# Kernel tuning notes

Hardware: AMD Instinct MI355X
Metric: run time of the kernel (lower is better)

The kernel has to match this reference:

```python
import jax, jax.numpy as jnp
import numpy as np

B, S, T, H, E, V = 64, 512, 12, 256, 256, 50000


def _xavier(key, shape):
    lim = np.sqrt(6.0 / (shape[0] + shape[1]))
    return jax.random.uniform(key, shape, jnp.float32, -lim, lim)


def setup_inputs() -> dict:
    key = jax.random.key(0)
    ks = jax.random.split(key, 14)
    return {
        "input_ids": jax.random.randint(ks[0], (B, S), 0, V),
        "tree_ids": jax.random.randint(ks[1], (B, T, S), 0, S),
        "tree_ids_r": jax.random.randint(ks[2], (B, T, S), 0, S),
        "tree_ids_l": jax.random.randint(ks[3], (B, T, S), 0, S),
        "emb": _xavier(ks[4], (V, E)),
        "W_ioux": _xavier(ks[5], (E, 3 * H)),
        "b_ioux": jnp.zeros((3 * H,), jnp.float32),
        "U_iou_r": _xavier(ks[6], (H, 3 * H)),
        "U_iou_l": _xavier(ks[7], (H, 3 * H)),
        "W_f": _xavier(ks[8], (E, H)),
        "b_f": jnp.zeros((H,), jnp.float32),
        "U_f0": _xavier(ks[9], (H, H)),
        "U_f1": _xavier(ks[10], (H, H)),
        "U_f2": _xavier(ks[11], (H, H)),
        "U_f3": _xavier(ks[12], (H, H)),
    }


def reference(input_ids, tree_ids, tree_ids_r, tree_ids_l, emb,
              W_ioux, b_ioux, U_iou_r, U_iou_l, W_f, b_f,
              U_f0, U_f1, U_f2, U_f3):
    x = emb[input_ids]                      # [B, S, E]
    Bn, Sn = x.shape[0], x.shape[1]
    Hn = U_f0.shape[0]
    bidx = jnp.arange(Bn)[:, None]          # [B, 1] batch index for scatter

    def take(a, idx):                       # gather along node dim: out[b,s]=a[b,idx[b,s]]
        return jnp.take_along_axis(a, idx[..., None], axis=1)

    iou_x = x @ W_ioux + b_ioux             # precompute; constant across steps
    f_x = x @ W_f + b_f

    def step(carry, ids):
        h, c = carry
        td, tr, tl = ids                    # each [B, S]
        # which parent nodes receive children this step (node 0 excluded)
        counts = jnp.zeros((Bn, Sn), x.dtype).at[bidx, td].add(1.0)
        mask = (counts.at[:, 0].set(0.0) > 0)[..., None]  # [B, S, 1]
        # scatter-add child hidden projections into parent iou preactivations
        iou = iou_x.at[bidx, tr].add(h @ U_iou_r)
        iou = iou.at[bidx, tl].add(h @ U_iou_l)
        i, o, u = jnp.split(iou, 3, axis=-1)
        i, o, u = jax.nn.sigmoid(i), jax.nn.sigmoid(o), jnp.tanh(u)
        # forget gate per child: gather parent fx and child-hidden projections
        f = jax.nn.sigmoid(take(f_x, td)
                           + take(h @ U_f0 + h @ U_f1, tr)
                           + take(h @ U_f2 + h @ U_f3, tl))
        c_new = (i * u).at[bidx, td].add(f * c)
        h_new = o * jnp.tanh(c_new)
        h = jnp.where(mask, h_new, h)
        c = jnp.where(mask, c_new, c)
        return (h, c), None

    h0 = jnp.zeros((Bn, Sn, Hn), x.dtype)
    ids = (jnp.swapaxes(tree_ids, 0, 1),
           jnp.swapaxes(tree_ids_r, 0, 1),
           jnp.swapaxes(tree_ids_l, 0, 1))   # [T, B, S]
    (h, c), _ = jax.lax.scan(step, (h0, h0), ids)

    roots = tree_ids[:, -1, :].max(axis=1)   # [B]
    h_root = h[jnp.arange(Bn), roots]        # [B, H]
    return h, c, h_root
```

## Files before the change

### kernel.cpp

```cpp
#include <hip/hip_runtime.h>
#include <stdint.h>

#define B_ 64
#define S_ 512
#define T_ 12
#define M_ (B_*S_)
#define NP_ 2048

typedef __attribute__((ext_vector_type(8))) short bf16x8;
typedef __attribute__((ext_vector_type(4))) float f32x4;

__device__ __forceinline__ uint16_t f2bf(float f){
  union { float f; uint32_t u; } x; x.f = f;
  uint32_t r = x.u + 0x7FFFu + ((x.u >> 16) & 1u);
  return (uint16_t)(r >> 16);
}
__device__ __forceinline__ float bf2f(uint16_t u){
  union { float f; uint32_t u; } x; x.u = ((uint32_t)u) << 16; return x.f;
}
__device__ __forceinline__ float sigm(float x){ return 1.0f/(1.0f + expf(-x)); }
__device__ __forceinline__ float4 bf4(const uint16_t* p){
  const ushort4 v = *reinterpret_cast<const ushort4*>(p);
  return make_float4(bf2f(v.x), bf2f(v.y), bf2f(v.z), bf2f(v.w));
}

__device__ __forceinline__ void gload16(const uint16_t* g, uint16_t* l){
  __builtin_amdgcn_global_load_lds(
      (const __attribute__((address_space(1))) uint32_t*)g,
      (__attribute__((address_space(3))) uint32_t*)l, 16, 0, 0);
}

__global__ void zero16(uint4* __restrict__ p, long n16){
  const long i = (long)blockIdx.x * 256 + threadIdx.x;
  if (i < n16) p[i] = make_uint4(0,0,0,0);
}
__global__ void bf16_to_f32(const uint16_t* __restrict__ src, float* __restrict__ dst, long n){
  const long i = ((long)blockIdx.x * 256 + threadIdx.x) * 4;
  if (i + 3 < n) {
    const float4 o = bf4(src + i);
    *reinterpret_cast<float4*>(dst + i) = o;
  }
}

__global__ void build_ucatT(const float* __restrict__ Ur, const float* __restrict__ Ul,
                            const float* __restrict__ f0, const float* __restrict__ f1,
                            const float* __restrict__ f2, const float* __restrict__ f3,
                            uint16_t* __restrict__ UcatT){
  const int idx = blockIdx.x * 256 + threadIdx.x;
  const int n = idx >> 8, k = idx & 255;
  float v;
  if (n < 768)        v = Ur[k*768 + n];
  else if (n < 1536)  v = Ul[k*768 + (n-768)];
  else if (n < 1792) { int j = n-1536; v = f0[k*256+j] + f1[k*256+j]; }
  else               { int j = n-1792; v = f2[k*256+j] + f3[k*256+j]; }
  UcatT[(long)n*256 + k] = f2bf(v);
}

__global__ void build_wallT(const float* __restrict__ Wioux, const float* __restrict__ Wf,
                            uint16_t* __restrict__ WT){
  const int idx = blockIdx.x * 256 + threadIdx.x;
  const int n = idx >> 8, k = idx & 255;
  const float v = (n < 768) ? Wioux[(long)k*768 + n] : Wf[(long)k*256 + (n-768)];
  WT[(long)n*256 + k] = f2bf(v);
}

__global__ void gather_embg(const float* __restrict__ emb, const int* __restrict__ ids,
                            uint16_t* __restrict__ out){
  const int wave = threadIdx.x >> 6, lane = threadIdx.x & 63;
  const long row = (long)blockIdx.x*4 + wave;
  const long rid = (long)ids[row];
  const float4 v = *reinterpret_cast<const float4*>(emb + rid*256 + lane*4);
  ushort4 o; o.x=f2bf(v.x); o.y=f2bf(v.y); o.z=f2bf(v.z); o.w=f2bf(v.w);
  *reinterpret_cast<ushort4*>(out + row*256 + lane*4) = o;
}

__global__ __launch_bounds__(256)
void gemm_pipe(const uint16_t* __restrict__ A, const uint16_t* __restrict__ BT,
               const float* __restrict__ bias, const float* __restrict__ bias2, int split,
               uint16_t* __restrict__ C, int N, int NT)
{
  __shared__ __align__(16) uint16_t smem[16384];
  const int tid = threadIdx.x, lane = tid & 63, wave = tid >> 6;
  const int wr = wave >> 1, wc = wave & 1;
  const int id = blockIdx.x, rx = id & 7, q = id >> 3;
  const int mt = rx + 8*(q / NT);
  const int nt = q % NT;
  const long m0 = (long)mt * 128;
  const int  n0 = nt * 128;

  const int rl0 = wave*32 + (lane >> 2);
  const int rl1 = rl0 + 16;
  const int sg0 = (lane & 3) ^ ((rl0 >> 1) & 3);
  const int sg1 = (lane & 3) ^ ((rl1 >> 1) & 3);
  const uint16_t* ga0 = A + (m0 + rl0)*256 + sg0*8;
  const uint16_t* ga1 = A + (m0 + rl1)*256 + sg1*8;
  const uint16_t* gb0 = BT + (long)(n0 + rl0)*256 + sg0*8;
  const uint16_t* gb1 = BT + (long)(n0 + rl1)*256 + sg1*8;

  f32x4 acc[4][4];
  #pragma unroll
  for (int i=0;i<4;i++)
    #pragma unroll
    for (int j=0;j<4;j++) acc[i][j] = (f32x4){0.f,0.f,0.f,0.f};

  const int l15 = lane & 15, lseg = lane >> 4;
  int aoff[4], boff[4];
  #pragma unroll
  for (int i=0;i<4;i++){ const int m = wr*64 + i*16 + l15; aoff[i] = m*32 + ((lseg ^ ((m>>1)&3))<<3); }
  #pragma unroll
  for (int j=0;j<4;j++){ const int n = wc*64 + j*16 + l15; boff[j] = n*32 + ((lseg ^ ((n>>1)&3))<<3); }

  #define STAGE(tile, buf) {                                   \
    const int ks_ = (tile)*32;                                 \
    uint16_t* a_ = &smem[(buf)*4096 + wave*1024];              \
    uint16_t* b_ = &smem[8192 + (buf)*4096 + wave*1024];       \
    gload16(ga0 + ks_, a_); gload16(ga1 + ks_, a_ + 512);      \
    gload16(gb0 + ks_, b_); gload16(gb1 + ks_, b_ + 512);      \
  }

  STAGE(0, 0)
  STAGE(1, 1)

  #pragma unroll
  for (int tt = 0; tt < 8; ++tt) {
    if (tt < 7) asm volatile("s_waitcnt vmcnt(4)" ::: "memory");
    else        asm volatile("s_waitcnt vmcnt(0)" ::: "memory");
    __builtin_amdgcn_s_barrier();
    const int cb = tt & 1;
    bf16x8 af[4], bfv[4];
    #pragma unroll
    for (int i=0;i<4;i++) af[i]  = *reinterpret_cast<const bf16x8*>(&smem[cb*4096 + aoff[i]]);
    #pragma unroll
    for (int j=0;j<4;j++) bfv[j] = *reinterpret_cast<const bf16x8*>(&smem[8192 + cb*4096 + boff[j]]);
    __builtin_amdgcn_s_setprio(1);
    #pragma unroll
    for (int i=0;i<4;i++)
      #pragma unroll
      for (int j=0;j<4;j++)
        acc[i][j] = __builtin_amdgcn_mfma_f32_16x16x32_bf16(af[i], bfv[j], acc[i][j], 0, 0, 0);
    __builtin_amdgcn_s_setprio(0);
    if (tt < 6) {
      __builtin_amdgcn_s_barrier();
      STAGE(tt + 2, cb)
    }
  }
  #undef STAGE

  __syncthreads();
  const int rquad = lane >> 4;
  const int rowq = tid >> 4;
  const int cseg = tid & 15;
  float bv[4];
  #pragma unroll
  for (int j=0;j<4;j++){
    const int col = n0 + wc*64 + j*16 + l15;
    bv[j] = bias ? ((col < split) ? bias[col] : bias2[col - split]) : 0.0f;
  }
  #pragma unroll
  for (int half = 0; half < 2; ++half) {
    if (wr == half) {
      #pragma unroll
      for (int i=0;i<4;i++)
        #pragma unroll
        for (int j=0;j<4;j++)
          #pragma unroll
          for (int r=0;r<4;r++)
            smem[(i*16 + rquad*4 + r)*136 + wc*64 + j*16 + l15] = f2bf(acc[i][j][r] + bv[j]);
    }
    __syncthreads();
    #pragma unroll
    for (int it=0; it<4; ++it) {
      const int r2 = it*16 + rowq;
      const uint4 v = *reinterpret_cast<const uint4*>(&smem[r2*136 + cseg*8]);
      *reinterpret_cast<uint4*>(C + (m0 + half*64 + r2)*N + n0 + cseg*8) = v;
    }
    __syncthreads();
  }
}

__global__ void build_csr(const int* __restrict__ td_g, const int* __restrict__ tr_g,
                          const int* __restrict__ tl_g,
                          int* __restrict__ csr_off, int* __restrict__ csr_val){
  const int t = blockIdx.x >> 6;
  const int b = blockIdx.x & 63;
  __shared__ int ids[S_];
  __shared__ int cnt[S_];
  __shared__ int off[S_];
  __shared__ int chc[8][S_];
  const int s = threadIdx.x;
  const int q = s >> 6;
  const int* srcs[3] = {td_g, tr_g, tl_g};
  for (int arr = 0; arr < 3; ++arr) {
    const int myid = srcs[arr][((long)b*T_ + t)*S_ + s];
    ids[s] = myid;
    cnt[s] = 0;
    #pragma unroll
    for (int qq=0; qq<8; qq++) chc[qq][s] = 0;
    __syncthreads();
    atomicAdd(&cnt[myid], 1);
    atomicAdd(&chc[q][myid], 1);
    __syncthreads();
    int rank = 0;
    for (int qq = 0; qq < q; ++qq) rank += chc[qq][myid];
    for (int i = q*64; i < s; ++i) rank += (ids[i] == myid) ? 1 : 0;
    off[s] = cnt[s];
    __syncthreads();
    for (int w = 1; w < S_; w <<= 1){
      const int v = (s >= w) ? off[s-w] : 0;
      __syncthreads();
      off[s] += v;
      __syncthreads();
    }
    const long base = (((long)arr*T_ + t)*B_ + b);
    int* offs = csr_off + base*(S_+1);
    int* vals = csr_val + base*S_;
    offs[s] = off[s] - cnt[s];
    if (s == S_-1) offs[S_] = off[s];
    vals[(off[myid] - cnt[myid]) + rank] = s;
    __syncthreads();
  }
}

__global__ __launch_bounds__(256)
void t0_update(uint16_t* __restrict__ h, uint16_t* __restrict__ c_out,
               const uint16_t* __restrict__ ioufx, const int* __restrict__ csr_off)
{
  const int wave = threadIdx.x >> 6, lane = threadIdx.x & 63;
  const long bs = (long)blockIdx.x*4 + wave;
  const int b = (int)(bs >> 9), s = (int)(bs & 511);
  const int j = lane * 4;
  const int* off_td = csr_off + (long)b*(S_+1);
  if (s == 0 || off_td[s+1] <= off_td[s]) return;
  const long ib = bs*1024;
  const float4 ai = bf4(ioufx + ib + j);
  const float4 ao = bf4(ioufx + ib + 256 + j);
  const float4 au = bf4(ioufx + ib + 512 + j);
  float4 cacc;
  cacc.x = sigm(ai.x)*tanhf(au.x); cacc.y = sigm(ai.y)*tanhf(au.y);
  cacc.z = sigm(ai.z)*tanhf(au.z); cacc.w = sigm(ai.w)*tanhf(au.w);
  ushort4 ho, co;
  ho.x = f2bf(sigm(ao.x)*tanhf(cacc.x)); ho.y = f2bf(sigm(ao.y)*tanhf(cacc.y));
  ho.z = f2bf(sigm(ao.z)*tanhf(cacc.z)); ho.w = f2bf(sigm(ao.w)*tanhf(cacc.w));
  co.x = f2bf(cacc.x); co.y = f2bf(cacc.y); co.z = f2bf(cacc.z); co.w = f2bf(cacc.w);
  *reinterpret_cast<ushort4*>(h + bs*256 + j) = ho;
  *reinterpret_cast<ushort4*>(c_out + bs*256 + j) = co;
}

__global__ __launch_bounds__(256)
void step_update(uint16_t* __restrict__ h,
                 const uint16_t* __restrict__ c_in, uint16_t* __restrict__ c_out,
                 const uint16_t* __restrict__ P,
                 const uint16_t* __restrict__ ioufx,
                 const int* __restrict__ csr_off, const int* __restrict__ csr_val,
                 const int* __restrict__ tr_g, const int* __restrict__ tl_g,
                 int t, int row0)
{
  const int wave = threadIdx.x >> 6, lane = threadIdx.x & 63;
  const int id = blockIdx.x, rx = id & 7, q = id >> 3;
  const int b_local = rx + 8*(q >> 7);
  const int rg = q & 127;
  const long bs = (long)row0 + b_local*512 + rg*4 + wave;
  const int b = (int)(bs >> 9), s = (int)(bs & 511);
  const int j = lane * 4;

  const int* off_td = csr_off + (((long)0*T_ + t)*B_ + b)*(S_+1);
  const int td0 = off_td[s], td1 = off_td[s+1];
  const bool masked = (s != 0) && (td1 > td0);
  if (!masked) {
    *reinterpret_cast<ushort4*>(c_out + bs*256 + j) =
        *reinterpret_cast<const ushort4*>(c_in + bs*256 + j);
    return;
  }
  const int* off_tr = csr_off + (((long)1*T_ + t)*B_ + b)*(S_+1);
  const int* off_tl = csr_off + (((long)2*T_ + t)*B_ + b)*(S_+1);
  const int* val_td = csr_val + (((long)0*T_ + t)*B_ + b)*S_;
  const int* val_tr = csr_val + (((long)1*T_ + t)*B_ + b)*S_;
  const int* val_tl = csr_val + (((long)2*T_ + t)*B_ + b)*S_;

  const long lbase = (long)(b<<9) - row0;

  const long ib = bs*1024;
  float4 ai = bf4(ioufx + ib + j);
  float4 ao = bf4(ioufx + ib + 256 + j);
  float4 au = bf4(ioufx + ib + 512 + j);
  for (int p = off_tr[s]; p < off_tr[s+1]; ++p) {
    const long pr = (lbase + val_tr[p]) * NP_;
    const float4 x = bf4(P + pr + j), y = bf4(P + pr + 256 + j), z = bf4(P + pr + 512 + j);
    ai.x+=x.x; ai.y+=x.y; ai.z+=x.z; ai.w+=x.w;
    ao.x+=y.x; ao.y+=y.y; ao.z+=y.z; ao.w+=y.w;
    au.x+=z.x; au.y+=z.y; au.z+=z.z; au.w+=z.w;
  }
  for (int p = off_tl[s]; p < off_tl[s+1]; ++p) {
    const long pr = (lbase + val_tl[p]) * NP_;
    const float4 x = bf4(P + pr + 768 + j), y = bf4(P + pr + 1024 + j), z = bf4(P + pr + 1280 + j);
    ai.x+=x.x; ai.y+=x.y; ai.z+=x.z; ai.w+=x.w;
    ao.x+=y.x; ao.y+=y.y; ao.z+=y.z; ao.w+=y.w;
    au.x+=z.x; au.y+=z.y; au.z+=z.z; au.w+=z.w;
  }
  float4 cacc;
  cacc.x = sigm(ai.x)*tanhf(au.x); cacc.y = sigm(ai.y)*tanhf(au.y);
  cacc.z = sigm(ai.z)*tanhf(au.z); cacc.w = sigm(ai.w)*tanhf(au.w);
  const float4 fxv = bf4(ioufx + ib + 768 + j);
  const int* trrow = tr_g + ((long)b*T_ + t)*S_;
  const int* tlrow = tl_g + ((long)b*T_ + t)*S_;
  for (int p = td0; p < td1; ++p) {
    const int sp = val_td[p];
    const long prr = (lbase + trrow[sp]) * NP_ + 1536;
    const long prl = (lbase + tlrow[sp]) * NP_ + 1792;
    const float4 pa = bf4(P + prr + j), pb = bf4(P + prl + j);
    const float4 cv = bf4(c_in + ((long)(b<<9) + sp)*256 + j);
    cacc.x += sigm(fxv.x + pa.x + pb.x) * cv.x;
    cacc.y += sigm(fxv.y + pa.y + pb.y) * cv.y;
    cacc.z += sigm(fxv.z + pa.z + pb.z) * cv.z;
    cacc.w += sigm(fxv.w + pa.w + pb.w) * cv.w;
  }
  ushort4 ho, co;
  ho.x = f2bf(sigm(ao.x) * tanhf(cacc.x));
  ho.y = f2bf(sigm(ao.y) * tanhf(cacc.y));
  ho.z = f2bf(sigm(ao.z) * tanhf(cacc.z));
  ho.w = f2bf(sigm(ao.w) * tanhf(cacc.w));
  co.x = f2bf(cacc.x); co.y = f2bf(cacc.y); co.z = f2bf(cacc.z); co.w = f2bf(cacc.w);
  *reinterpret_cast<ushort4*>(h + bs*256 + j) = ho;
  *reinterpret_cast<ushort4*>(c_out + bs*256 + j) = co;
}

__global__ void root_kernel(const uint16_t* __restrict__ h, const int* __restrict__ td_g,
                            float* __restrict__ out_root){
  const int b = blockIdx.x;
  __shared__ int red[256];
  const int* td = td_g + ((long)b*T_ + (T_-1))*S_;
  int m = 0;
  for (int s = threadIdx.x; s < S_; s += 256) m = max(m, td[s]);
  red[threadIdx.x] = m; __syncthreads();
  for (int w = 128; w > 0; w >>= 1){
    if (threadIdx.x < w) red[threadIdx.x] = max(red[threadIdx.x], red[threadIdx.x+w]);
    __syncthreads();
  }
  const int root = red[0];
  out_root[b*256 + threadIdx.x] = bf2f(h[((long)b*512 + root)*256 + threadIdx.x]);
}

extern "C" void kernel_launch(void* const* d_in, const int* in_sizes, int n_in,
                              void* d_out, int out_size, void* d_ws, size_t ws_size,
                              hipStream_t stream) {
  const int*   input_ids  = (const int*)  d_in[0];
  const int*   tree_ids   = (const int*)  d_in[1];
  const int*   tree_ids_r = (const int*)  d_in[2];
  const int*   tree_ids_l = (const int*)  d_in[3];
  const float* emb        = (const float*)d_in[4];
  const float* W_ioux     = (const float*)d_in[5];
  const float* b_ioux     = (const float*)d_in[6];
  const float* W_f        = (const float*)d_in[9];
  const float* b_f        = (const float*)d_in[10];
  float* out = (float*)d_out;

  size_t woff = 0;
  auto alloc = [&](size_t bytes)->char*{
    char* p = (char*)d_ws + woff; woff += (bytes + 255) & ~(size_t)255; return p;
  };
  uint16_t* ioufx  = (uint16_t*)alloc((size_t)M_*1024*2);
  uint16_t* hA     = (uint16_t*)alloc((size_t)M_*256*2);
  uint16_t* cA     = (uint16_t*)alloc((size_t)M_*256*2);
  uint16_t* cB     = (uint16_t*)alloc((size_t)M_*256*2);
  int* csr_off     = (int*)     alloc((size_t)3*T_*B_*(S_+1)*4);
  int* csr_val     = (int*)     alloc((size_t)3*T_*B_*S_*4);
  uint16_t* UcatT  = (uint16_t*)alloc((size_t)NP_*256*2);
  uint16_t* WallT  = (uint16_t*)alloc((size_t)1024*256*2);
  int CB = 64;
  while (CB > 8 && woff + (size_t)CB*S_*NP_*2 > ws_size) CB >>= 1;
  uint16_t* P      = (uint16_t*)alloc((size_t)CB*S_*NP_*2);
  uint16_t* embg   = P;

  build_ucatT<<<2048, 256, 0, stream>>>((const float*)d_in[7], (const float*)d_in[8],
      (const float*)d_in[11], (const float*)d_in[12], (const float*)d_in[13], (const float*)d_in[14],
      UcatT);
  build_wallT<<<1024, 256, 0, stream>>>(W_ioux, W_f, WallT);
  gather_embg<<<M_/4, 256, 0, stream>>>(emb, input_ids, embg);
  gemm_pipe<<<(M_/128)*8, 256, 0, stream>>>(embg, WallT, b_ioux, b_f, 768, ioufx, 1024, 8);
  build_csr<<<T_*B_, S_, 0, stream>>>(tree_ids, tree_ids_r, tree_ids_l, csr_off, csr_val);
  zero16<<<12288, 256, 0, stream>>>((uint4*)hA, 3145728L);

  uint16_t *cc = cA, *cn = cB;
  t0_update<<<M_/4, 256, 0, stream>>>(hA, cn, ioufx, csr_off);
  { uint16_t* tc = cc; cc = cn; cn = tc; }
  for (int t = 1; t < T_; ++t) {
    for (int b0 = 0; b0 < B_; b0 += CB) {
      const int row0 = b0 * S_;
      const int Mc   = CB * S_;
      gemm_pipe<<<(Mc/128)*16, 256, 0, stream>>>(hA + (long)row0*256, UcatT,
                                                 nullptr, nullptr, 0, P, NP_, 16);
      step_update<<<CB*128, 256, 0, stream>>>(hA, cc, cn, P, ioufx,
                                              csr_off, csr_val, tree_ids_r, tree_ids_l,
                                              t, row0);
    }
    uint16_t* tc = cc; cc = cn; cn = tc;
  }

  bf16_to_f32<<<8192, 256, 0, stream>>>(hA, out, (long)M_*256);
  bf16_to_f32<<<8192, 256, 0, stream>>>(cc, out + (long)M_*256, (long)M_*256);
  root_kernel<<<B_, 256, 0, stream>>>(hA, tree_ids, out + 2L*M_*256);
}
```

Baseline: 1.127 ms.

## Store step GEMM output in blocked tiles, two N-tiles per block

Adds a dedicated per-step GEMM kernel that writes the child-hidden projection P in contiguous 128x128 tile blocks instead of a row-major 2048-wide matrix. Each block computes two N tiles, reusing its A rows, with a grid ordering that groups M tiles. The update kernel's gather addressing is rewritten to this blocked layout so each half-wave reads a contiguous 256-byte tile row. The goal is better write locality and a larger per-block workload, at the cost of more complex indexing and halving the grid size.

Result: slower. 1.530 ms (+35.7%).

```diff
diff --git a/kernel.cpp b/kernel.cpp
--- a/kernel.cpp
+++ b/kernel.cpp
@@ -175,6 +175,112 @@
       *reinterpret_cast<uint4*>(C + (m0 + half*64 + r2)*N + n0 + cseg*8) = v;
     }
     __syncthreads();
+  }
+}
+
+__global__ __launch_bounds__(256)
+void gemm_step_blk(const uint16_t* __restrict__ A, const uint16_t* __restrict__ BT,
+                   uint16_t* __restrict__ P)
+{
+  __shared__ __align__(16) uint16_t smem[16384];
+  const int tid = threadIdx.x, lane = tid & 63, wave = tid >> 6;
+  const int wr = wave >> 1, wc = wave & 1;
+  const int mt8 = gridDim.x >> 6;
+  const int id = blockIdx.x, rx = id & 7, q = id >> 3;
+  const int ntp = q / mt8;
+  const int mq  = q - ntp*mt8;
+  const int mt  = rx + 8*mq;
+  const long m0 = (long)mt * 128;
+
+  const int rl0 = wave*32 + (lane >> 2);
+  const int rl1 = rl0 + 16;
+  const int sg0 = (lane & 3) ^ ((rl0 >> 1) & 3);
+  const int sg1 = (lane & 3) ^ ((rl1 >> 1) & 3);
+  const uint16_t* ga0 = A + (m0 + rl0)*256 + sg0*8;
+  const uint16_t* ga1 = A + (m0 + rl1)*256 + sg1*8;
+
+  const int l15 = lane & 15, lseg = lane >> 4;
+  int aoff[4], boff[4];
+  #pragma unroll
+  for (int i=0;i<4;i++){ const int m = wr*64 + i*16 + l15; aoff[i] = m*32 + ((lseg ^ ((m>>1)&3))<<3); }
+  #pragma unroll
+  for (int j=0;j<4;j++){ const int n = wc*64 + j*16 + l15; boff[j] = n*32 + ((lseg ^ ((n>>1)&3))<<3); }
+
+  const int rquad = lane >> 4;
+  const int rowq = tid >> 4;
+  const int cseg = tid & 15;
+
+  #pragma unroll
+  for (int t2 = 0; t2 < 2; ++t2) {
+    const int nt = ntp + t2*8;
+    const int n0 = nt * 128;
+    const uint16_t* gb0 = BT + (long)(n0 + rl0)*256 + sg0*8;
+    const uint16_t* gb1 = BT + (long)(n0 + rl1)*256 + sg1*8;
+
+    f32x4 acc[4][4];
+    #pragma unroll
+    for (int i=0;i<4;i++)
+      #pragma unroll
+      for (int j=0;j<4;j++) acc[i][j] = (f32x4){0.f,0.f,0.f,0.f};
+
+    #define STAGE(tile, buf) {                                   \
+      const int ks_ = (tile)*32;                                 \
+      uint16_t* a_ = &smem[(buf)*4096 + wave*1024];              \
+      uint16_t* b_ = &smem[8192 + (buf)*4096 + wave*1024];       \
+      gload16(ga0 + ks_, a_); gload16(ga1 + ks_, a_ + 512);      \
+      gload16(gb0 + ks_, b_); gload16(gb1 + ks_, b_ + 512);      \
+    }
+
+    STAGE(0, 0)
+    STAGE(1, 1)
+
+    #pragma unroll
+    for (int tt = 0; tt < 8; ++tt) {
+      if (tt < 7) asm volatile("s_waitcnt vmcnt(4)" ::: "memory");
+      else        asm volatile("s_waitcnt vmcnt(0)" ::: "memory");
+      __builtin_amdgcn_s_barrier();
+      const int cb = tt & 1;
+      bf16x8 af[4], bfv[4];
+      #pragma unroll
+      for (int i=0;i<4;i++) af[i]  = *reinterpret_cast<const bf16x8*>(&smem[cb*4096 + aoff[i]]);
+      #pragma unroll
+      for (int j=0;j<4;j++) bfv[j] = *reinterpret_cast<const bf16x8*>(&smem[8192 + cb*4096 + boff[j]]);
+      __builtin_amdgcn_s_setprio(1);
+      #pragma unroll
+      for (int i=0;i<4;i++)
+        #pragma unroll
+        for (int j=0;j<4;j++)
+          acc[i][j] = __builtin_amdgcn_mfma_f32_16x16x32_bf16(af[i], bfv[j], acc[i][j], 0, 0, 0);
+      __builtin_amdgcn_s_setprio(0);
+      if (tt < 6) {
+        __builtin_amdgcn_s_barrier();
+        STAGE(tt + 2, cb)
+      }
+    }
+    #undef STAGE
+
+    __syncthreads();
+    uint16_t* dst = P + ((long)(mt*16 + nt) << 14);
+    #pragma unroll
+    for (int half = 0; half < 2; ++half) {
+      if (wr == half) {
+        #pragma unroll
+        for (int i=0;i<4;i++)
+          #pragma unroll
+          for (int j=0;j<4;j++)
+            #pragma unroll
+            for (int r=0;r<4;r++)
+              smem[(i*16 + rquad*4 + r)*136 + wc*64 + j*16 + l15] = f2bf(acc[i][j][r]);
+      }
+      __syncthreads();
+      #pragma unroll
+      for (int it=0; it<4; ++it) {
+        const int r2 = it*16 + rowq;
+        const uint4 v = *reinterpret_cast<const uint4*>(&smem[r2*136 + cseg*8]);
+        *reinterpret_cast<uint4*>(dst + (half*64 + r2)*128 + cseg*8) = v;
+      }
+      __syncthreads();
+    }
   }
 }
 
@@ -279,20 +385,24 @@
 
   const long lbase = (long)(b<<9) - row0;
 
+  const int seg_add = lane >> 5;
+  const int cix = (lane & 31) * 4;
+  #define PP(lr, s8) (P + ((((long)((lr)>>7)<<4) + (s8) + seg_add)<<14) + (((lr)&127)<<7) + cix)
+
   const long ib = bs*1024;
   float4 ai = bf4(ioufx + ib + j);
   float4 ao = bf4(ioufx + ib + 256 + j);
   float4 au = bf4(ioufx + ib + 512 + j);
   for (int p = off_tr[s]; p < off_tr[s+1]; ++p) {
-    const long pr = (lbase + val_tr[p]) * NP_;
-    const float4 x = bf4(P + pr + j), y = bf4(P + pr + 256 + j), z = bf4(P + pr + 512 + j);
+    const long lr = lbase + val_tr[p];
+    const float4 x = bf4(PP(lr,0)), y = bf4(PP(lr,2)), z = bf4(PP(lr,4));
     ai.x+=x.x; ai.y+=x.y; ai.z+=x.z; ai.w+=x.w;
     ao.x+=y.x; ao.y+=y.y; ao.z+=y.z; ao.w+=y.w;
     au.x+=z.x; au.y+=z.y; au.z+=z.z; au.w+=z.w;
   }
   for (int p = off_tl[s]; p < off_tl[s+1]; ++p) {
-    const long pr = (lbase + val_tl[p]) * NP_;
-    const float4 x = bf4(P + pr + 768 + j), y = bf4(P + pr + 1024 + j), z = bf4(P + pr + 1280 + j);
+    const long lr = lbase + val_tl[p];
+    const float4 x = bf4(PP(lr,6)), y = bf4(PP(lr,8)), z = bf4(PP(lr,10));
     ai.x+=x.x; ai.y+=x.y; ai.z+=x.z; ai.w+=x.w;
     ao.x+=y.x; ao.y+=y.y; ao.z+=y.z; ao.w+=y.w;
     au.x+=z.x; au.y+=z.y; au.z+=z.z; au.w+=z.w;
@@ -305,15 +415,16 @@
   const int* tlrow = tl_g + ((long)b*T_ + t)*S_;
   for (int p = td0; p < td1; ++p) {
     const int sp = val_td[p];
-    const long prr = (lbase + trrow[sp]) * NP_ + 1536;
-    const long prl = (lbase + tlrow[sp]) * NP_ + 1792;
-    const float4 pa = bf4(P + prr + j), pb = bf4(P + prl + j);
+    const long lrr = lbase + trrow[sp];
+    const long lrl = lbase + tlrow[sp];
+    const float4 pa = bf4(PP(lrr,12)), pb = bf4(PP(lrl,14));
     const float4 cv = bf4(c_in + ((long)(b<<9) + sp)*256 + j);
     cacc.x += sigm(fxv.x + pa.x + pb.x) * cv.x;
     cacc.y += sigm(fxv.y + pa.y + pb.y) * cv.y;
     cacc.z += sigm(fxv.z + pa.z + pb.z) * cv.z;
     cacc.w += sigm(fxv.w + pa.w + pb.w) * cv.w;
   }
+  #undef PP
   ushort4 ho, co;
   ho.x = f2bf(sigm(ao.x) * tanhf(cacc.x));
   ho.y = f2bf(sigm(ao.y) * tanhf(cacc.y));
@@ -387,8 +498,7 @@
     for (int b0 = 0; b0 < B_; b0 += CB) {
       const int row0 = b0 * S_;
       const int Mc   = CB * S_;
-      gemm_pipe<<<(Mc/128)*16, 256, 0, stream>>>(hA + (long)row0*256, UcatT,
-                                                 nullptr, nullptr, 0, P, NP_, 16);
+      gemm_step_blk<<<Mc/16, 256, 0, stream>>>(hA + (long)row0*256, UcatT, P);
       step_update<<<CB*128, 256, 0, stream>>>(hA, cc, cn, P, ioufx,
                                               csr_off, csr_val, tree_ids_r, tree_ids_l,
                                               t, row0);
```
